# Kernel tuning notes

Hardware: AMD Instinct MI355X
Metric: run time of the kernel (lower is better)

Reference implementation:

```python
import jax, jax.numpy as jnp
import numpy as np
from jax import lax

B, CIN, H, W = 8, 64, 128, 128
COUT, K, STRIDE, PAD = 128, 3, 1, 1
NLEV = 256  # 2**activation_bits == 2**weight_bits


def setup_inputs() -> dict:
    key = jax.random.key(0)
    kx, kw = jax.random.split(key)
    x = jax.random.uniform(kx, (B, CIN, H, W), dtype=jnp.float32)
    weight = jax.random.normal(kw, (COUT, CIN, K, K), dtype=jnp.float32)
    bias = jnp.zeros((COUT,), dtype=jnp.float32)
    return {"x": x, "weight": weight, "bias": bias}


def _lut_table(weight):
    # quantized weights in [0, 255], integer-valued
    qw = jnp.clip(jnp.round(weight * (NLEV - 1)), 0, NLEV - 1).astype(jnp.int32)
    iv = jnp.arange(NLEV, dtype=jnp.int32)
    # emulate torch .to(int16) wraparound (qw*i can exceed 32767)
    lut = (qw[..., None] * iv).astype(jnp.int16)          # [O, C, K, K, 256]
    # the original sums pcilt over its (c,p,q) dims for EVERY patch entry;
    # precollapse those dims: T[i, o] = sum_{c,p,q} lut[o,c,p,q,i]
    T = lut.astype(jnp.int32).sum(axis=(1, 2, 3))          # [O, 256]
    return T.T                                             # [256, O]


def reference(x, weight, bias):
    T = _lut_table(weight)                                 # [256, COUT]
    xq = jnp.clip(jnp.round(x * (NLEV - 1)), 0, NLEV - 1).astype(jnp.int32)
    xp = jnp.pad(xq, ((0, 0), (0, 0), (PAD, PAD), (PAD, PAD)))  # zero-pad; T[:,0]=0 matches
    xc = jnp.moveaxis(xp, 1, 0)                            # [CIN, B, Hp, Wp]

    # accumulate per-pixel channel sum of LUT rows: A[b,h,w,o] = sum_c T[x[b,c,h,w], o]
    A0 = jnp.zeros((xp.shape[0], xp.shape[2], xp.shape[3], COUT), dtype=jnp.int32)

    def body(acc, ch):
        return acc + T[ch], None

    A, _ = lax.scan(body, A0, xc)                          # [B, Hp, Wp, COUT]

    # k x k sliding-window sum over spatial dims = sum over all patch entries
    out = lax.reduce_window(A.astype(jnp.float32), 0.0, lax.add,
                            (1, K, K, 1), (1, STRIDE, STRIDE, 1), 'VALID')
    out = jnp.moveaxis(out, 3, 1) + bias[None, :, None, None]  # [B, COUT, OH, OW]
    return out
```

## Files before the change

### kernel.cpp

```cpp
#include <hip/hip_runtime.h>

#define CIN   64
#define HW    128
#define COUT  128
#define TH    8
#define TW    32
#define NITER 12
#define NTHR  512
#define HSTR  144
#define SLOT  (34 * HSTR)
#define H3SL  (32 * HSTR)

#define HM_OFF    0
#define H3_OFF    19584
#define SXR_OFF   38016
#define SX9_OFF   39616
#define LDS_BYTES 40896

typedef int v4i __attribute__((ext_vector_type(4)));

__device__ __forceinline__ void wg_barrier() {
  asm volatile("s_waitcnt lgkmcnt(0)\n\ts_barrier" ::: "memory");
}

__device__ __forceinline__ int quad_sum(int v) {
  v += __builtin_amdgcn_mov_dpp(v, 0xB1, 0xF, 0xF, true);
  v += __builtin_amdgcn_mov_dpp(v, 0x4E, 0xF, 0xF, true);
  return v;
}
__device__ __forceinline__ int row16_sum(int v) {
  v = quad_sum(v);
  v += __builtin_amdgcn_mov_dpp(v, 0x114, 0xF, 0xF, true);
  v += __builtin_amdgcn_mov_dpp(v, 0x118, 0xF, 0xF, true);
  return v;
}

__global__ __launch_bounds__(512)
void build_tables(const float* __restrict__ weight, int* __restrict__ W_tab,
                  char* __restrict__ Kt_g) {
  __shared__ int qw_s[576];
  __shared__ int red_s[144];
  const int o = blockIdx.x;
  const int t = threadIdx.x;
  for (int j = t; j < 576; j += 512) {
    float w = weight[o * 576 + j];
    int q = (int)rintf(w * 255.f);
    qw_s[j] = q < 0 ? 0 : (q > 255 ? 255 : q);
  }
  __syncthreads();
  const int v = t >> 2, part = t & 3;
  const int i = 128 + v;
  int cnt = 0;
  const int j0 = part * 144;
  for (int j = j0; j < j0 + 144; ++j) cnt += (qw_s[j] * i) > 32767 ? 1 : 0;
  cnt = quad_sum(cnt);
  if (part == 0) Kt_g[o * 128 + v] = (char)(cnt - 128);
  if (t < 144)
    red_s[t] = qw_s[t * 4] + qw_s[t * 4 + 1] + qw_s[t * 4 + 2] + qw_s[t * 4 + 3];
  __syncthreads();
  if (t == 0) {
    int s = 0;
    for (int kk = 0; kk < 144; ++kk) s += red_s[kk];
    W_tab[o] = s;
  }
}

__global__ __launch_bounds__(NTHR, 4)
void pcilt_main(const float* __restrict__ x, const float* __restrict__ bias,
                const int* __restrict__ W_tab, const char* __restrict__ Kt_g,
                float* __restrict__ out) {
  __shared__ uint4 ldsv[LDS_BYTES / 16];
  char* ldsb = (char*)ldsv;
  unsigned char* HmB = (unsigned char*)(ldsb + HM_OFF);
  unsigned char* H3B = (unsigned char*)(ldsb + H3_OFF);
  unsigned char* KtB = (unsigned char*)(ldsb + H3_OFF);
  int* SxR = (int*)(ldsb + SXR_OFF);
  int* Sx9 = (int*)(ldsb + SX9_OFF);

  const int t   = (int)threadIdx.x;
  const int bid = (int)blockIdx.x;
  const int b  = bid & 7;
  const int k  = bid >> 3;
  const int h0 = (k >> 2) * TH;
  const int w0 = (k & 3) * TW;

  for (int i = t; i < 4096; i += NTHR)
    ((unsigned int*)KtB)[i] = ((const unsigned int*)Kt_g)[i];
  {
    const uint4 z4 = make_uint4(0, 0, 0, 0);
    for (int i = t; i < SLOT / 16; i += NTHR) ((uint4*)HmB)[i] = z4;
  }

  const int l    = t & 15;
  const int slot = t >> 4;
  const int wv   = t >> 6;
  const int kq   = (t >> 4) & 3;
  const int Mt   = wv >> 2;
  const int Nh   = wv & 3;
  const int o0   = Nh * 32 + l;

  const float wfo0 = (float)W_tab[o0],      bio0 = bias[o0];
  const float wfo1 = (float)W_tab[o0 + 16], bio1 = bias[o0 + 16];

  wg_barrier();

  v4i bfr[2][2];
#pragma unroll
  for (int nt = 0; nt < 2; ++nt)
#pragma unroll
    for (int k64 = 0; k64 < 2; ++k64)
      bfr[nt][k64] = *(const v4i*)(KtB + (o0 + nt * 16) * 128 + k64 * 64 + kq * 16);

  unsigned int qd[10], qd2[10];
  {
    const float* xb = x + ((size_t)b * CIN + l * 4) * (HW * HW);
    const size_t cs = (size_t)HW * HW;
    const int ix0 = w0 + slot - 1;
    const int ix0c = ix0 < 0 ? 0 : (ix0 > 127 ? 127 : ix0);
    const bool wok0 = (ix0 >= 0) && (ix0 < HW);
    const int ix1 = w0 + slot + 1;
    const int ix1c = ix1 > 127 ? 127 : ix1;
    const bool wok1 = ix1 < HW;
    const bool dual = slot >= 30;
#pragma unroll
    for (int row = 0; row < 10; ++row) {
      const int iy = h0 + row - 1;
      const int iyc = iy < 0 ? 0 : (iy > 127 ? 127 : iy);
      const bool rok = (iy >= 0) && (iy < HW);
      {
        const float* xp = xb + (size_t)iyc * HW + ix0c;
        const bool ok = rok && wok0;
        float f0 = xp[0], f1 = xp[cs], f2 = xp[2 * cs], f3 = xp[3 * cs];
        f0 = ok ? f0 : 0.f; f1 = ok ? f1 : 0.f; f2 = ok ? f2 : 0.f; f3 = ok ? f3 : 0.f;
        int q0 = (int)rintf(f0 * 255.f); q0 = q0 < 0 ? 0 : (q0 > 255 ? 255 : q0);
        int q1 = (int)rintf(f1 * 255.f); q1 = q1 < 0 ? 0 : (q1 > 255 ? 255 : q1);
        int q2 = (int)rintf(f2 * 255.f); q2 = q2 < 0 ? 0 : (q2 > 255 ? 255 : q2);
        int q3 = (int)rintf(f3 * 255.f); q3 = q3 < 0 ? 0 : (q3 > 255 ? 255 : q3);
        qd[row] = (unsigned)q0 | ((unsigned)q1 << 8) | ((unsigned)q2 << 16) | ((unsigned)q3 << 24);
        int pk = (((q0 > 128) + (q1 > 128) + (q2 > 128) + (q3 > 128)) << 20) +
                 (q0 + q1 + q2 + q3);
        pk = row16_sum(pk);
        if (l == 15) SxR[row * 40 + slot] = pk;
      }
      {
        const float* xp = xb + (size_t)iyc * HW + ix1c;
        const bool ok = dual && rok && wok1;
        float f0 = ok ? xp[0] : 0.f, f1 = ok ? xp[cs] : 0.f;
        float f2 = ok ? xp[2 * cs] : 0.f, f3 = ok ? xp[3 * cs] : 0.f;
        int q0 = (int)rintf(f0 * 255.f); q0 = q0 < 0 ? 0 : (q0 > 255 ? 255 : q0);
        int q1 = (int)rintf(f1 * 255.f); q1 = q1 < 0 ? 0 : (q1 > 255 ? 255 : q1);
        int q2 = (int)rintf(f2 * 255.f); q2 = q2 < 0 ? 0 : (q2 > 255 ? 255 : q2);
        int q3 = (int)rintf(f3 * 255.f); q3 = q3 < 0 ? 0 : (q3 > 255 ? 255 : q3);
        qd2[row] = (unsigned)q0 | ((unsigned)q1 << 8) | ((unsigned)q2 << 16) | ((unsigned)q3 << 24);
        int pk = (((q0 > 128) + (q1 > 128) + (q2 > 128) + (q3 > 128)) << 20) +
                 (q0 + q1 + q2 + q3);
        pk = row16_sum(pk);
        if (dual && l == 15) SxR[row * 40 + slot + 2] = pk;
      }
    }
  }
  wg_barrier();

#define HISTD(dw, px, Hc)                                                      \
  {                                                                            \
    unsigned char* hp = (Hc) + (px)*HSTR;                                      \
    const unsigned b0 = (dw) & 255u, b1 = ((dw) >> 8) & 255u;                  \
    const unsigned b2 = ((dw) >> 16) & 255u, b3 = (dw) >> 24;                  \
    if (b0 > 128u) { unsigned v = b0 - 128u; atomicAdd((unsigned*)(hp + ((v >> 2) << 2)), 1u << ((v & 3) * 8)); } \
    if (b1 > 128u) { unsigned v = b1 - 128u; atomicAdd((unsigned*)(hp + ((v >> 2) << 2)), 1u << ((v & 3) * 8)); } \
    if (b2 > 128u) { unsigned v = b2 - 128u; atomicAdd((unsigned*)(hp + ((v >> 2) << 2)), 1u << ((v & 3) * 8)); } \
    if (b3 > 128u) { unsigned v = b3 - 128u; atomicAdd((unsigned*)(hp + ((v >> 2) << 2)), 1u << ((v & 3) * 8)); } \
  }

#pragma unroll
  for (int r = 0; r < NITER; ++r) {
    if (r <= 9) {
      unsigned char* Hc = HmB + (r & 3) * SLOT;
      HISTD(qd[r], slot, Hc);
      if (slot >= 30) HISTD(qd2[r], slot + 2, Hc);
    }
    if (r == 0 && t < 256) {
      const int j = t >> 5, L = t & 31;
      int v9 = 0;
#pragma unroll
      for (int q = 0; q < 3; ++q) {
        const int* sr = &SxR[(j + q) * 40 + L];
        v9 += sr[0] + sr[1] + sr[2];
      }
      Sx9[j * 40 + L] = v9;
    }
    if (r >= 1 && r <= 10 && t < 256) {
      const int px = t & 31, ch = (t >> 5) * 16;
      const unsigned char* hs = HmB + ((r - 1) & 3) * SLOT + px * HSTR + ch;
      const uint4 a0 = *(const uint4*)hs;
      const uint4 a1 = *(const uint4*)(hs + HSTR);
      const uint4 a2 = *(const uint4*)(hs + 2 * HSTR);
      uint4 s;
      s.x = a0.x + a1.x + a2.x; s.y = a0.y + a1.y + a2.y;
      s.z = a0.z + a1.z + a2.z; s.w = a0.w + a1.w + a2.w;
      *(uint4*)(H3B + ((r - 1) & 3) * H3SL + px * HSTR + ch) = s;
    }
    if (r >= 4) {
      v4i acc0 = (v4i){0, 0, 0, 0}, acc1 = (v4i){0, 0, 0, 0};
#pragma unroll
      for (int st = 0; st < 3; ++st) {
        const unsigned char* Hs = H3B + ((r - 4 + st) & 3) * H3SL +
                                  (Mt * 16 + l) * HSTR + kq * 16;
#pragma unroll
        for (int k64 = 0; k64 < 2; ++k64) {
          const v4i a = *(const v4i*)(Hs + k64 * 64);
          acc0 = __builtin_amdgcn_mfma_i32_16x16x64_i8(a, bfr[0][k64], acc0, 0, 0, 0);
          acc1 = __builtin_amdgcn_mfma_i32_16x16x64_i8(a, bfr[1][k64], acc1, 0, 0, 0);
        }
      }
      const int j = r - 4, h = h0 + j, px0 = Mt * 16 + kq * 4;
      const v4i s9 = *(const v4i*)&Sx9[j * 40 + px0];
      float4 u0, u1;
#pragma unroll
      for (int rg = 0; rg < 4; ++rg) {
        const int sx = s9[rg] & 0xFFFFF;
        const int sh = s9[rg] >> 20;
        ((float*)&u0)[rg] = (float)sx * wfo0 - 65536.f * (float)(acc0[rg] + (sh << 7)) + bio0;
        ((float*)&u1)[rg] = (float)sx * wfo1 - 65536.f * (float)(acc1[rg] + (sh << 7)) + bio1;
      }
      float* op = out + (((size_t)b * COUT + o0) * HW + h) * HW + w0 + px0;
      *(float4*)op = u0;
      *(float4*)(op + 16 * (size_t)(HW * HW)) = u1;
    }
    if (r <= 8 && wv >= 4 && wv < 6) {
      uint4* Hn = (uint4*)(HmB + ((r + 1) & 3) * SLOT);
      const uint4 z4 = make_uint4(0, 0, 0, 0);
      for (int i2 = t - 256; i2 < SLOT / 16; i2 += 128) Hn[i2] = z4;
    }
    wg_barrier();
  }
}

extern "C" void kernel_launch(void* const* d_in, const int* in_sizes, int n_in,
                              void* d_out, int out_size, void* d_ws, size_t ws_size,
                              hipStream_t stream) {
  const float* x      = (const float*)d_in[0];
  const float* weight = (const float*)d_in[1];
  const float* bias   = (const float*)d_in[2];
  float* out = (float*)d_out;

  int*  W_tab = (int*)d_ws;
  char* Kt_g  = (char*)d_ws + 512;

  build_tables<<<128, 512, 0, stream>>>(weight, W_tab, Kt_g);

  pcilt_main<<<512, NTHR, 0, stream>>>(x, bias, W_tab, Kt_g, out);
}
```

Before: 48.97 us.

## Switch to single-wave workgroups with small 2x16 tiles and no barriers

Replaces the 512-thread workgroup covering an 8x32 tile with a 64-thread single-wavefront workgroup covering a 2x16 output tile, launched as 4096 blocks. Because each block is one wave, all s_barrier synchronisation is dropped, and the LDS footprint shrinks from about 40KB to 10KB so more blocks can be resident. Each wave now computes all 128 output channels with 8 MFMA accumulators, reading the weight fragments directly from global memory instead of staging them in LDS. The cost is more redundant halo loads and quantisation of input rows (4 rows loaded per 2 output rows, 18 columns per 16), plus serialised histogram atomics within one wave.

```diff
diff --git a/kernel.cpp b/kernel.cpp
--- a/kernel.cpp
+++ b/kernel.cpp
@@ -1,27 +1,17 @@
 #include <hip/hip_runtime.h>
 
-#define CIN   64
 #define HW    128
 #define COUT  128
-#define TH    8
-#define TW    32
-#define NITER 12
-#define NTHR  512
 #define HSTR  144
-#define SLOT  (34 * HSTR)
-#define H3SL  (32 * HSTR)
-
-#define HM_OFF    0
-#define H3_OFF    19584
-#define SXR_OFF   38016
-#define SX9_OFF   39616
-#define LDS_BYTES 40896
+#define H3SL  (16 * HSTR)
+
+#define RAW_OFF   0
+#define H3_OFF    2592
+#define SXR_OFF   9504
+#define SXH_OFF   9824
+#define LDS_BYTES 10080
 
 typedef int v4i __attribute__((ext_vector_type(4)));
-
-__device__ __forceinline__ void wg_barrier() {
-  asm volatile("s_waitcnt lgkmcnt(0)\n\ts_barrier" ::: "memory");
-}
 
 __device__ __forceinline__ int quad_sum(int v) {
   v += __builtin_amdgcn_mov_dpp(v, 0xB1, 0xF, 0xF, true);
@@ -65,174 +55,151 @@
   }
 }
 
-__global__ __launch_bounds__(NTHR, 4)
+__global__ __launch_bounds__(64, 4)
 void pcilt_main(const float* __restrict__ x, const float* __restrict__ bias,
                 const int* __restrict__ W_tab, const char* __restrict__ Kt_g,
                 float* __restrict__ out) {
   __shared__ uint4 ldsv[LDS_BYTES / 16];
   char* ldsb = (char*)ldsv;
-  unsigned char* HmB = (unsigned char*)(ldsb + HM_OFF);
+  unsigned char* RAW = (unsigned char*)(ldsb + RAW_OFF);
   unsigned char* H3B = (unsigned char*)(ldsb + H3_OFF);
-  unsigned char* KtB = (unsigned char*)(ldsb + H3_OFF);
   int* SxR = (int*)(ldsb + SXR_OFF);
-  int* Sx9 = (int*)(ldsb + SX9_OFF);
+  int* SxH = (int*)(ldsb + SXH_OFF);
 
   const int t   = (int)threadIdx.x;
   const int bid = (int)blockIdx.x;
-  const int b  = bid & 7;
-  const int k  = bid >> 3;
-  const int h0 = (k >> 2) * TH;
-  const int w0 = (k & 3) * TW;
-
-  for (int i = t; i < 4096; i += NTHR)
-    ((unsigned int*)KtB)[i] = ((const unsigned int*)Kt_g)[i];
-  {
-    const uint4 z4 = make_uint4(0, 0, 0, 0);
-    for (int i = t; i < SLOT / 16; i += NTHR) ((uint4*)HmB)[i] = z4;
-  }
-
-  const int l    = t & 15;
-  const int slot = t >> 4;
-  const int wv   = t >> 6;
-  const int kq   = (t >> 4) & 3;
-  const int Mt   = wv >> 2;
-  const int Nh   = wv & 3;
-  const int o0   = Nh * 32 + l;
-
-  const float wfo0 = (float)W_tab[o0],      bio0 = bias[o0];
-  const float wfo1 = (float)W_tab[o0 + 16], bio1 = bias[o0 + 16];
-
-  wg_barrier();
-
-  v4i bfr[2][2];
-#pragma unroll
-  for (int nt = 0; nt < 2; ++nt)
-#pragma unroll
-    for (int k64 = 0; k64 < 2; ++k64)
-      bfr[nt][k64] = *(const v4i*)(KtB + (o0 + nt * 16) * 128 + k64 * 64 + kq * 16);
-
-  unsigned int qd[10], qd2[10];
-  {
-    const float* xb = x + ((size_t)b * CIN + l * 4) * (HW * HW);
-    const size_t cs = (size_t)HW * HW;
-    const int ix0 = w0 + slot - 1;
-    const int ix0c = ix0 < 0 ? 0 : (ix0 > 127 ? 127 : ix0);
-    const bool wok0 = (ix0 >= 0) && (ix0 < HW);
-    const int ix1 = w0 + slot + 1;
-    const int ix1c = ix1 > 127 ? 127 : ix1;
-    const bool wok1 = ix1 < HW;
-    const bool dual = slot >= 30;
-#pragma unroll
-    for (int row = 0; row < 10; ++row) {
-      const int iy = h0 + row - 1;
-      const int iyc = iy < 0 ? 0 : (iy > 127 ? 127 : iy);
-      const bool rok = (iy >= 0) && (iy < HW);
-      {
-        const float* xp = xb + (size_t)iyc * HW + ix0c;
-        const bool ok = rok && wok0;
-        float f0 = xp[0], f1 = xp[cs], f2 = xp[2 * cs], f3 = xp[3 * cs];
-        f0 = ok ? f0 : 0.f; f1 = ok ? f1 : 0.f; f2 = ok ? f2 : 0.f; f3 = ok ? f3 : 0.f;
-        int q0 = (int)rintf(f0 * 255.f); q0 = q0 < 0 ? 0 : (q0 > 255 ? 255 : q0);
-        int q1 = (int)rintf(f1 * 255.f); q1 = q1 < 0 ? 0 : (q1 > 255 ? 255 : q1);
-        int q2 = (int)rintf(f2 * 255.f); q2 = q2 < 0 ? 0 : (q2 > 255 ? 255 : q2);
-        int q3 = (int)rintf(f3 * 255.f); q3 = q3 < 0 ? 0 : (q3 > 255 ? 255 : q3);
-        qd[row] = (unsigned)q0 | ((unsigned)q1 << 8) | ((unsigned)q2 << 16) | ((unsigned)q3 << 24);
-        int pk = (((q0 > 128) + (q1 > 128) + (q2 > 128) + (q3 > 128)) << 20) +
-                 (q0 + q1 + q2 + q3);
-        pk = row16_sum(pk);
-        if (l == 15) SxR[row * 40 + slot] = pk;
-      }
-      {
-        const float* xp = xb + (size_t)iyc * HW + ix1c;
-        const bool ok = dual && rok && wok1;
-        float f0 = ok ? xp[0] : 0.f, f1 = ok ? xp[cs] : 0.f;
-        float f2 = ok ? xp[2 * cs] : 0.f, f3 = ok ? xp[3 * cs] : 0.f;
-        int q0 = (int)rintf(f0 * 255.f); q0 = q0 < 0 ? 0 : (q0 > 255 ? 255 : q0);
-        int q1 = (int)rintf(f1 * 255.f); q1 = q1 < 0 ? 0 : (q1 > 255 ? 255 : q1);
-        int q2 = (int)rintf(f2 * 255.f); q2 = q2 < 0 ? 0 : (q2 > 255 ? 255 : q2);
-        int q3 = (int)rintf(f3 * 255.f); q3 = q3 < 0 ? 0 : (q3 > 255 ? 255 : q3);
-        qd2[row] = (unsigned)q0 | ((unsigned)q1 << 8) | ((unsigned)q2 << 16) | ((unsigned)q3 << 24);
-        int pk = (((q0 > 128) + (q1 > 128) + (q2 > 128) + (q3 > 128)) << 20) +
-                 (q0 + q1 + q2 + q3);
-        pk = row16_sum(pk);
-        if (dual && l == 15) SxR[row * 40 + slot + 2] = pk;
-      }
-    }
-  }
-  wg_barrier();
-
-#define HISTD(dw, px, Hc)                                                      \
-  {                                                                            \
-    unsigned char* hp = (Hc) + (px)*HSTR;                                      \
-    const unsigned b0 = (dw) & 255u, b1 = ((dw) >> 8) & 255u;                  \
-    const unsigned b2 = ((dw) >> 16) & 255u, b3 = (dw) >> 24;                  \
-    if (b0 > 128u) { unsigned v = b0 - 128u; atomicAdd((unsigned*)(hp + ((v >> 2) << 2)), 1u << ((v & 3) * 8)); } \
-    if (b1 > 128u) { unsigned v = b1 - 128u; atomicAdd((unsigned*)(hp + ((v >> 2) << 2)), 1u << ((v & 3) * 8)); } \
-    if (b2 > 128u) { unsigned v = b2 - 128u; atomicAdd((unsigned*)(hp + ((v >> 2) << 2)), 1u << ((v & 3) * 8)); } \
-    if (b3 > 128u) { unsigned v = b3 - 128u; atomicAdd((unsigned*)(hp + ((v >> 2) << 2)), 1u << ((v & 3) * 8)); } \
-  }
-
-#pragma unroll
-  for (int r = 0; r < NITER; ++r) {
-    if (r <= 9) {
-      unsigned char* Hc = HmB + (r & 3) * SLOT;
-      HISTD(qd[r], slot, Hc);
-      if (slot >= 30) HISTD(qd2[r], slot + 2, Hc);
-    }
-    if (r == 0 && t < 256) {
-      const int j = t >> 5, L = t & 31;
-      int v9 = 0;
-#pragma unroll
-      for (int q = 0; q < 3; ++q) {
-        const int* sr = &SxR[(j + q) * 40 + L];
-        v9 += sr[0] + sr[1] + sr[2];
-      }
-      Sx9[j * 40 + L] = v9;
-    }
-    if (r >= 1 && r <= 10 && t < 256) {
-      const int px = t & 31, ch = (t >> 5) * 16;
-      const unsigned char* hs = HmB + ((r - 1) & 3) * SLOT + px * HSTR + ch;
-      const uint4 a0 = *(const uint4*)hs;
-      const uint4 a1 = *(const uint4*)(hs + HSTR);
-      const uint4 a2 = *(const uint4*)(hs + 2 * HSTR);
+  const int b   = bid & 7;
+  const int rem = bid >> 3;
+  const int h0  = (rem >> 3) * 2;
+  const int w0  = (rem & 7) * 16;
+
+  const int g  = t >> 4;
+  const int q  = t & 15;
+
+  const uint4 z4 = make_uint4(0, 0, 0, 0);
+#pragma unroll
+  for (int p = 0; p < 3; ++p) {
+    const int i = p * 64 + t;
+    if (i < 162) ((uint4*)RAW)[i] = z4;
+  }
+
+  float Wf[8], Bf[8];
+#pragma unroll
+  for (int nt = 0; nt < 8; ++nt) {
+    Wf[nt] = (float)W_tab[nt * 16 + q];
+    Bf[nt] = bias[nt * 16 + q];
+  }
+  v4i Bfr[8];
+#pragma unroll
+  for (int nt = 0; nt < 8; ++nt)
+    Bfr[nt] = *(const v4i*)(Kt_g + (nt * 16 + q) * 128 + g * 16);
+
+  const size_t cs16k = (size_t)HW * HW;
+
+#pragma unroll
+  for (int r = 0; r < 4; ++r) {
+    const int iy  = h0 + r - 1;
+    const int iyc = iy < 0 ? 0 : (iy > 127 ? 127 : iy);
+    const bool rok = (iy >= 0) && (iy < HW);
+#pragma unroll
+    for (int p = 0; p < 5; ++p) {
+      const int px = p * 4 + g;
+      const bool pv = px < 18;
+      const int ix = w0 + px - 1;
+      const int ixc = ix < 0 ? 0 : (ix > 127 ? 127 : ix);
+      const bool ok = pv && rok && (ix >= 0) && (ix < HW);
+      const float* xp = x + ((size_t)b * 64 + q * 4) * cs16k + (size_t)iyc * HW + ixc;
+      float f0 = xp[0], f1 = xp[cs16k], f2 = xp[2 * cs16k], f3 = xp[3 * cs16k];
+      f0 = ok ? f0 : 0.f; f1 = ok ? f1 : 0.f; f2 = ok ? f2 : 0.f; f3 = ok ? f3 : 0.f;
+      int q0 = (int)rintf(f0 * 255.f); q0 = q0 < 0 ? 0 : (q0 > 255 ? 255 : q0);
+      int q1 = (int)rintf(f1 * 255.f); q1 = q1 < 0 ? 0 : (q1 > 255 ? 255 : q1);
+      int q2 = (int)rintf(f2 * 255.f); q2 = q2 < 0 ? 0 : (q2 > 255 ? 255 : q2);
+      int q3 = (int)rintf(f3 * 255.f); q3 = q3 < 0 ? 0 : (q3 > 255 ? 255 : q3);
+      if (pv) {
+        unsigned char* hp = RAW + px * HSTR;
+        if (q0 > 128) { int v = q0 - 128; atomicAdd((unsigned*)(hp + ((v >> 2) << 2)), 1u << ((v & 3) * 8)); }
+        if (q1 > 128) { int v = q1 - 128; atomicAdd((unsigned*)(hp + ((v >> 2) << 2)), 1u << ((v & 3) * 8)); }
+        if (q2 > 128) { int v = q2 - 128; atomicAdd((unsigned*)(hp + ((v >> 2) << 2)), 1u << ((v & 3) * 8)); }
+        if (q3 > 128) { int v = q3 - 128; atomicAdd((unsigned*)(hp + ((v >> 2) << 2)), 1u << ((v & 3) * 8)); }
+      }
+      int pk = (((q0 > 128) + (q1 > 128) + (q2 > 128) + (q3 > 128)) << 20) +
+               (q0 + q1 + q2 + q3);
+      pk = row16_sum(pk);
+      if (pv && q == 15) SxR[r * 20 + px] = pk;
+    }
+    asm volatile("s_waitcnt lgkmcnt(0)" ::: "memory");
+#pragma unroll
+    for (int pp = 0; pp < 2; ++pp) {
+      const int task = pp * 64 + t;
+      const int px = task >> 3, ch = (task & 7) * 16;
+      const unsigned char* rp = RAW + px * HSTR + ch;
+      const uint4 a0 = *(const uint4*)rp;
+      const uint4 a1 = *(const uint4*)(rp + HSTR);
+      const uint4 a2 = *(const uint4*)(rp + 2 * HSTR);
       uint4 s;
       s.x = a0.x + a1.x + a2.x; s.y = a0.y + a1.y + a2.y;
       s.z = a0.z + a1.z + a2.z; s.w = a0.w + a1.w + a2.w;
-      *(uint4*)(H3B + ((r - 1) & 3) * H3SL + px * HSTR + ch) = s;
-    }
-    if (r >= 4) {
-      v4i acc0 = (v4i){0, 0, 0, 0}, acc1 = (v4i){0, 0, 0, 0};
+      *(uint4*)(H3B + (r % 3) * H3SL + px * HSTR + ch) = s;
+    }
+    if (t < 16) {
+      SxH[r * 16 + t] = SxR[r * 20 + t] + SxR[r * 20 + t + 1] + SxR[r * 20 + t + 2];
+    }
+    if (r < 3) {
+#pragma unroll
+      for (int p = 0; p < 3; ++p) {
+        const int i = p * 64 + t;
+        if (i < 162) ((uint4*)RAW)[i] = z4;
+      }
+    }
+    if (r >= 2) {
+      const int j = r - 2;
+      asm volatile("s_waitcnt lgkmcnt(0)" ::: "memory");
+      v4i acc[8];
+#pragma unroll
+      for (int nt = 0; nt < 8; ++nt) acc[nt] = (v4i){0, 0, 0, 0};
 #pragma unroll
       for (int st = 0; st < 3; ++st) {
-        const unsigned char* Hs = H3B + ((r - 4 + st) & 3) * H3SL +
-                                  (Mt * 16 + l) * HSTR + kq * 16;
-#pragma unroll
-        for (int k64 = 0; k64 < 2; ++k64) {
-          const v4i a = *(const v4i*)(Hs + k64 * 64);
-          acc0 = __builtin_amdgcn_mfma_i32_16x16x64_i8(a, bfr[0][k64], acc0, 0, 0, 0);
-          acc1 = __builtin_amdgcn_mfma_i32_16x16x64_i8(a, bfr[1][k64], acc1, 0, 0, 0);
+        const v4i a = *(const v4i*)(H3B + ((j + st) % 3) * H3SL + q * HSTR + g * 16);
+#pragma unroll
+        for (int nt = 0; nt < 8; ++nt)
+          acc[nt] = __builtin_amdgcn_mfma_i32_16x16x64_i8(a, Bfr[nt], acc[nt], 0, 0, 0);
+      }
+#pragma unroll
+      for (int nt = 0; nt < 8; ++nt)
+        Bfr[nt] = *(const v4i*)(Kt_g + (nt * 16 + q) * 128 + 64 + g * 16);
+#pragma unroll
+      for (int st = 0; st < 3; ++st) {
+        const v4i a = *(const v4i*)(H3B + ((j + st) % 3) * H3SL + q * HSTR + 64 + g * 16);
+#pragma unroll
+        for (int nt = 0; nt < 8; ++nt)
+          acc[nt] = __builtin_amdgcn_mfma_i32_16x16x64_i8(a, Bfr[nt], acc[nt], 0, 0, 0);
+      }
+      if (j == 0) {
+#pragma unroll
+        for (int nt = 0; nt < 8; ++nt)
+          Bfr[nt] = *(const v4i*)(Kt_g + (nt * 16 + q) * 128 + g * 16);
+      }
+      v4i s9 = (v4i){0, 0, 0, 0};
+#pragma unroll
+      for (int dy = 0; dy < 3; ++dy) {
+        const v4i sv = *(const v4i*)&SxH[(j + dy) * 16 + g * 4];
+        s9[0] += sv[0]; s9[1] += sv[1]; s9[2] += sv[2]; s9[3] += sv[3];
+      }
+      const int h = h0 + j;
+#pragma unroll
+      for (int nt = 0; nt < 8; ++nt) {
+        const int o = nt * 16 + q;
+        float4 u;
+#pragma unroll
+        for (int rg = 0; rg < 4; ++rg) {
+          const int sx = s9[rg] & 0xFFFFF;
+          const int sh = s9[rg] >> 20;
+          ((float*)&u)[rg] = (float)sx * Wf[nt] -
+                             65536.f * (float)(acc[nt][rg] + (sh << 7)) + Bf[nt];
         }
-      }
-      const int j = r - 4, h = h0 + j, px0 = Mt * 16 + kq * 4;
-      const v4i s9 = *(const v4i*)&Sx9[j * 40 + px0];
-      float4 u0, u1;
-#pragma unroll
-      for (int rg = 0; rg < 4; ++rg) {
-        const int sx = s9[rg] & 0xFFFFF;
-        const int sh = s9[rg] >> 20;
-        ((float*)&u0)[rg] = (float)sx * wfo0 - 65536.f * (float)(acc0[rg] + (sh << 7)) + bio0;
-        ((float*)&u1)[rg] = (float)sx * wfo1 - 65536.f * (float)(acc1[rg] + (sh << 7)) + bio1;
-      }
-      float* op = out + (((size_t)b * COUT + o0) * HW + h) * HW + w0 + px0;
-      *(float4*)op = u0;
-      *(float4*)(op + 16 * (size_t)(HW * HW)) = u1;
-    }
-    if (r <= 8 && wv >= 4 && wv < 6) {
-      uint4* Hn = (uint4*)(HmB + ((r + 1) & 3) * SLOT);
-      const uint4 z4 = make_uint4(0, 0, 0, 0);
-      for (int i2 = t - 256; i2 < SLOT / 16; i2 += 128) Hn[i2] = z4;
-    }
-    wg_barrier();
+        *(float4*)(out + ((size_t)(b * COUT + o) * HW + h) * HW + w0 + g * 4) = u;
+      }
+    }
   }
 }
 
@@ -249,5 +216,5 @@
 
   build_tables<<<128, 512, 0, stream>>>(weight, W_tab, Kt_g);
 
-  pcilt_main<<<512, NTHR, 0, stream>>>(x, bias, W_tab, Kt_g, out);
-}
+  pcilt_main<<<4096, 64, 0, stream>>>(x, bias, W_tab, Kt_g, out);
+}
```

New measurement: 84.85 us. 73.3% more time.
